# Kernel tuning notes

Hardware: AMD Instinct MI355X
Metric: run time of the kernel (lower is better)

The kernel has to match this reference:

```python
import jax, jax.numpy as jnp
import numpy as np
import math

B = 2        # batch
S = 4095     # input sequence (cls token makes L = 4096)
F_IN = 32    # input feature size
D = 512      # d_model (hidden_size)
H = 8        # n_heads
E = D // H   # head dim = 64
DFF = 2048   # feedforward dim
NL = 2       # encoder layers
FACTOR = 5   # probsparse sampling factor
EPS = 1e-5


def setup_inputs() -> dict:
    key = jax.random.key(0)
    ks = jax.random.split(key, 16)

    def w(k, shape):
        return jax.random.normal(k, shape, dtype=jnp.float32) * 0.02

    inp = {}
    inp['x'] = jax.random.normal(ks[0], (B, S, F_IN), dtype=jnp.float32)
    inp['We'] = w(ks[1], (D, F_IN)); inp['be'] = jnp.zeros((D,), jnp.float32)
    inp['cls'] = jnp.zeros((1, 1, D), jnp.float32)
    inp['Wq'] = w(ks[2], (NL, D, D)); inp['bq'] = jnp.zeros((NL, D), jnp.float32)
    inp['Wk'] = w(ks[3], (NL, D, D)); inp['bk'] = jnp.zeros((NL, D), jnp.float32)
    inp['Wv'] = w(ks[4], (NL, D, D)); inp['bv'] = jnp.zeros((NL, D), jnp.float32)
    inp['Wo'] = w(ks[5], (NL, D, D)); inp['bo'] = jnp.zeros((NL, D), jnp.float32)
    inp['g1'] = jnp.ones((NL, D), jnp.float32); inp['b1'] = jnp.zeros((NL, D), jnp.float32)
    inp['g2'] = jnp.ones((NL, D), jnp.float32); inp['b2'] = jnp.zeros((NL, D), jnp.float32)
    inp['W1'] = w(ks[6], (NL, DFF, D)); inp['bf1'] = jnp.zeros((NL, DFF), jnp.float32)
    inp['W2'] = w(ks[7], (NL, D, DFF)); inp['bf2'] = jnp.zeros((NL, D), jnp.float32)
    inp['Wf'] = w(ks[8], (1, D)); inp['bf'] = jnp.zeros((1,), jnp.float32)
    return inp


def pos_encoding(L):
    # Sinusoidal positional encoding [L, D]
    pos = jnp.arange(L, dtype=jnp.float32)[:, None]
    div = jnp.exp(jnp.arange(0, D, 2, dtype=jnp.float32) * (-math.log(10000.0) / D))
    pe = jnp.zeros((L, D), jnp.float32)
    pe = pe.at[:, 0::2].set(jnp.sin(pos * div))
    pe = pe.at[:, 1::2].set(jnp.cos(pos * div))
    return pe


def layer_norm(x, g, b):
    mu = x.mean(-1, keepdims=True)
    var = ((x - mu) ** 2).mean(-1, keepdims=True)
    return (x - mu) / jnp.sqrt(var + EPS) * g + b


def prob_attention(q, k, v, rng):
    # q, k, v: [B, H, L, E]; mask_flag=False (encoder self-attention)
    b, h, L, e = q.shape
    u = min(FACTOR * int(np.ceil(np.log(L))), L)  # sample_k == n_top here (L_Q == L_K)
    idx = jax.random.randint(rng, (L, u), 0, L)   # random K sampling per query position
    Ks = k[:, :, idx, :]                          # [B,H,L,u,E] gather
    QKs = jnp.einsum('bhle,bhlue->bhlu', q, Ks)   # sampled scores
    M = QKs.max(-1) - QKs.sum(-1) / L             # sparsity measure [B,H,L]
    _, top = jax.lax.top_k(M, u)                  # active query indices [B,H,u]
    Qr = jnp.take_along_axis(q, top[..., None], axis=2)      # [B,H,u,E]
    scores = jnp.einsum('bhue,bhke->bhuk', Qr, k) / math.sqrt(e)
    attn = jax.nn.softmax(scores, axis=-1)
    ctx = jnp.broadcast_to(v.mean(axis=2, keepdims=True), (b, h, L, e))  # initial context = mean(V)
    upd = jnp.einsum('bhuk,bhke->bhue', attn, v)
    bi = jnp.arange(b)[:, None, None]
    hi = jnp.arange(h)[None, :, None]
    ctx = ctx.at[bi, hi, top].set(upd)            # scatter active-query contexts
    return ctx                                    # [B,H,L,E]


def attention_layer(x, Wq_, bq_, Wk_, bk_, Wv_, bv_, Wo_, bo_, rng):
    b, L, _ = x.shape
    q = (x @ Wq_.T + bq_).reshape(b, L, H, E).transpose(0, 2, 1, 3)
    k = (x @ Wk_.T + bk_).reshape(b, L, H, E).transpose(0, 2, 1, 3)
    v = (x @ Wv_.T + bv_).reshape(b, L, H, E).transpose(0, 2, 1, 3)
    ctx = prob_attention(q, k, v, rng)            # [B,H,L,E]
    out = ctx.transpose(0, 2, 1, 3).reshape(b, L, D)
    return out @ Wo_.T + bo_


def reference(x, We, be, cls, Wq, bq, Wk, bk, Wv, bv, Wo, bo, g1, b1, g2, b2, W1, bf1, W2, bf2, Wf, bf):
    h = x @ We.T + be                                            # [B,S,D]
    h = jnp.concatenate([jnp.broadcast_to(cls, (B, 1, D)), h], axis=1)  # prepend cls
    L = h.shape[1]
    h = h + pos_encoding(L)[None]
    for l in range(NL):
        rng = jax.random.fold_in(jax.random.key(42), l)
        a = attention_layer(h, Wq[l], bq[l], Wk[l], bk[l], Wv[l], bv[l], Wo[l], bo[l], rng)
        h = layer_norm(h + a, g1[l], b1[l])
        y = jax.nn.relu(h @ W1[l].T + bf1[l])
        y = y @ W2[l].T + bf2[l]
        h = layer_norm(h + y, g2[l], b2[l])
    return h[:, 0] @ Wf.T + bf  # cls-token prediction head [B,1]
```

## Files before the change

kernel.cpp:

```cpp
#include <hip/hip_runtime.h>
#include <hip/hip_bf16.h>
#include <math.h>
#include <stdint.h>

#define B 2
#define S 4095
#define LSEQ 4096
#define F_IN 32
#define D 512
#define H 8
#define E 64
#define DFF 2048
#define NL 2
#define U 45
#define EPSL 1e-5f
#define LU (LSEQ * U)
#define HALF_LU (LU / 2)
#define NS 32
#define SLICE 128

typedef __attribute__((ext_vector_type(8))) short short8;
typedef __attribute__((ext_vector_type(4))) float f32x4;

#define GLD(gp, lp)                                                            \
    __builtin_amdgcn_global_load_lds(                                          \
        (const __attribute__((address_space(1))) void*)(gp),                   \
        (__attribute__((address_space(3))) void*)(lp), 16, 0, 0)

__device__ __forceinline__ unsigned short bf16_bits(float f) {
    __hip_bfloat16 h = __float2bfloat16(f);
    return *(unsigned short*)&h;
}
__device__ __forceinline__ float bits_to_f32(unsigned short s) {
    union { uint32_t u; float f; } c;
    c.u = ((uint32_t)s) << 16;
    return c.f;
}
__device__ __forceinline__ unsigned long long mkey(float v, int index) {
    uint32_t u = __float_as_uint(v);
    uint32_t mono = (u & 0x80000000u) ? ~u : (u | 0x80000000u);
    return ((unsigned long long)mono << 32) | (uint32_t)(0xFFFFFFFFu - (uint32_t)index);
}

#define TF_BODY(k0, k1, c0, c1, o0, o1)                                        \
    do {                                                                       \
        uint32_t ks2 = (k0) ^ (k1) ^ 0x1BD11BDAu;                              \
        uint32_t x0 = (c0) + (k0), x1 = (c1) + (k1);                           \
        x0 += x1; x1 = ((x1 << 13) | (x1 >> 19)); x1 ^= x0;                    \
        x0 += x1; x1 = ((x1 << 15) | (x1 >> 17)); x1 ^= x0;                    \
        x0 += x1; x1 = ((x1 << 26) | (x1 >> 6));  x1 ^= x0;                    \
        x0 += x1; x1 = ((x1 << 6) | (x1 >> 26));  x1 ^= x0;                    \
        x0 += (k1); x1 += ks2 + 1u;                                            \
        x0 += x1; x1 = ((x1 << 17) | (x1 >> 15)); x1 ^= x0;                    \
        x0 += x1; x1 = ((x1 << 29) | (x1 >> 3));  x1 ^= x0;                    \
        x0 += x1; x1 = ((x1 << 16) | (x1 >> 16)); x1 ^= x0;                    \
        x0 += x1; x1 = ((x1 << 24) | (x1 >> 8));  x1 ^= x0;                    \
        x0 += ks2; x1 += (k0) + 2u;                                            \
        x0 += x1; x1 = ((x1 << 13) | (x1 >> 19)); x1 ^= x0;                    \
        x0 += x1; x1 = ((x1 << 15) | (x1 >> 17)); x1 ^= x0;                    \
        x0 += x1; x1 = ((x1 << 26) | (x1 >> 6));  x1 ^= x0;                    \
        x0 += x1; x1 = ((x1 << 6) | (x1 >> 26));  x1 ^= x0;                    \
        x0 += (k0); x1 += (k1) + 3u;                                           \
        x0 += x1; x1 = ((x1 << 17) | (x1 >> 15)); x1 ^= x0;                    \
        x0 += x1; x1 = ((x1 << 29) | (x1 >> 3));  x1 ^= x0;                    \
        x0 += x1; x1 = ((x1 << 16) | (x1 >> 16)); x1 ^= x0;                    \
        x0 += x1; x1 = ((x1 << 24) | (x1 >> 8));  x1 ^= x0;                    \
        x0 += (k1); x1 += ks2 + 4u;                                            \
        x0 += x1; x1 = ((x1 << 13) | (x1 >> 19)); x1 ^= x0;                    \
        x0 += x1; x1 = ((x1 << 15) | (x1 >> 17)); x1 ^= x0;                    \
        x0 += x1; x1 = ((x1 << 26) | (x1 >> 6));  x1 ^= x0;                    \
        x0 += x1; x1 = ((x1 << 6) | (x1 >> 26));  x1 ^= x0;                    \
        x0 += ks2; x1 += (k0) + 5u;                                            \
        (o0) = x0; (o1) = x1;                                                  \
    } while (0)

__device__ __forceinline__ void threefry_dev(uint32_t k0, uint32_t k1, uint32_t c0,
                                             uint32_t c1, uint32_t& o0, uint32_t& o1) {
    TF_BODY(k0, k1, c0, c1, o0, o1);
}
static void threefry_host(uint32_t k0, uint32_t k1, uint32_t c0, uint32_t c1,
                          uint32_t& o0, uint32_t& o1) {
    TF_BODY(k0, k1, c0, c1, o0, o1);
}

__global__ void prep_embed_kernel(const float* __restrict__ x, const float* __restrict__ We,
                                  __hip_bfloat16* __restrict__ xbf,
                                  __hip_bfloat16* __restrict__ webf) {
    int u = blockIdx.x * blockDim.x + threadIdx.x;
    const int NX = B * LSEQ * F_IN / 4;
    const int NW = D * F_IN / 4;
    if (u < NX) {
        int e0 = u * 4;
        int i = e0 & 31;
        int l = (e0 >> 5) & (LSEQ - 1);
        int b = e0 >> 17;
        union { unsigned short s[4]; uint2 w; } o;
        if (l == 0) {
            o.s[0] = o.s[1] = o.s[2] = o.s[3] = 0;
        } else {
            float4 v = *(const float4*)(x + ((size_t)b * S + (l - 1)) * F_IN + i);
            o.s[0] = bf16_bits(v.x); o.s[1] = bf16_bits(v.y);
            o.s[2] = bf16_bits(v.z); o.s[3] = bf16_bits(v.w);
        }
        ((uint2*)xbf)[u] = o.w;
    } else if (u < NX + NW) {
        int w = u - NX;
        float4 v = ((const float4*)We)[w];
        union { unsigned short s[4]; uint2 w2; } o;
        o.s[0] = bf16_bits(v.x); o.s[1] = bf16_bits(v.y);
        o.s[2] = bf16_bits(v.z); o.s[3] = bf16_bits(v.w);
        ((uint2*)webf)[w] = o.w2;
    }
}

__global__ __launch_bounds__(256) void gemm32(const unsigned short* __restrict__ A,
                                              const unsigned short* __restrict__ W,
                                              const float* __restrict__ bias,
                                              float* __restrict__ Cf,
                                              int M, int N, int K) {
    __shared__ unsigned short lds[2 * 128 * 32];
    unsigned short* As = lds;
    unsigned short* Bs = lds + 128 * 32;
    const int tid = threadIdx.x;
    const int m0 = blockIdx.y * 128, n0 = blockIdx.x * 128;
    const int wave = tid >> 6, lane = tid & 63;
    const int wm = (wave >> 1) * 64, wn = (wave & 1) * 64;
    const int quad = lane >> 4, m15 = lane & 15;
    const int srow = tid >> 2, scol = (tid & 3) * 8;
    f32x4 acc[4][4] = {};
    const unsigned short* Ag0 = A + (size_t)(m0 + srow) * K + scol;
    const unsigned short* Ag1 = A + (size_t)(m0 + srow + 64) * K + scol;
    const unsigned short* Wg0 = W + (size_t)(n0 + srow) * K + scol;
    const unsigned short* Wg1 = W + (size_t)(n0 + srow + 64) * K + scol;
    for (int k0 = 0; k0 < K; k0 += 32) {
        __syncthreads();
        GLD(Ag0 + k0, As + tid * 8);
        GLD(Ag1 + k0, As + 2048 + tid * 8);
        GLD(Wg0 + k0, Bs + tid * 8);
        GLD(Wg1 + k0, Bs + 2048 + tid * 8);
        __syncthreads();
        short8 af[4], bfr[4];
#pragma unroll
        for (int mi = 0; mi < 4; ++mi)
            af[mi] = *(const short8*)(As + (wm + mi * 16 + m15) * 32 + quad * 8);
#pragma unroll
        for (int ni = 0; ni < 4; ++ni)
            bfr[ni] = *(const short8*)(Bs + (wn + ni * 16 + m15) * 32 + quad * 8);
#pragma unroll
        for (int mi = 0; mi < 4; ++mi)
#pragma unroll
            for (int ni = 0; ni < 4; ++ni)
                acc[mi][ni] = __builtin_amdgcn_mfma_f32_16x16x32_bf16(
                    af[mi], bfr[ni], acc[mi][ni], 0, 0, 0);
    }
#pragma unroll
    for (int mi = 0; mi < 4; ++mi) {
        int mg = m0 + wm + mi * 16 + quad * 4;
#pragma unroll
        for (int ni = 0; ni < 4; ++ni) {
            int ng = n0 + wn + ni * 16 + m15;
            float bv = bias[ng];
#pragma unroll
            for (int r = 0; r < 4; ++r)
                Cf[(size_t)(mg + r) * N + ng] = acc[mi][ni][r] + bv;
        }
    }
}

__global__ void posenc_kernel(const float* __restrict__ emb, const float* __restrict__ cls,
                              __hip_bfloat16* __restrict__ hbf) {
    int gid = blockIdx.x * blockDim.x + threadIdx.x;
    if (gid >= B * LSEQ * D) return;
    int d = gid % D;
    int l = (gid / D) % LSEQ;
    float v = (l == 0) ? cls[d] : emb[gid];
    int i = d >> 1;
    float divv = expf((float)(2 * i) * (float)(-9.210340371976184 / 512.0));
    float ang = (float)l * divv;
    v += (d & 1) ? cosf(ang) : sinf(ang);
    hbf[gid] = __float2bfloat16(v);
}

__global__ void cast_weights_kernel(const float* __restrict__ Wq_l,
                                    const float* __restrict__ Wk_l,
                                    const float* __restrict__ Wv_l,
                                    const float* __restrict__ Wo_l,
                                    const float* __restrict__ W1_l,
                                    const float* __restrict__ W2_l,
                                    const float* __restrict__ bq_l,
                                    const float* __restrict__ bk_l,
                                    const float* __restrict__ bv_l,
                                    __hip_bfloat16* __restrict__ wqb,
                                    __hip_bfloat16* __restrict__ wkb,
                                    __hip_bfloat16* __restrict__ wvb,
                                    __hip_bfloat16* __restrict__ wob,
                                    __hip_bfloat16* __restrict__ w1b,
                                    __hip_bfloat16* __restrict__ w2b,
                                    float* __restrict__ qkvbias,
                                    unsigned char* __restrict__ flags) {
    const int SDD = D * D / 4;
    const int SFD = DFF * D / 4;
    const int CAST_N = 4 * SDD + 2 * SFD;
    int u = blockIdx.x * blockDim.x + threadIdx.x;
    if (u >= CAST_N) {
        int j = u - CAST_N;
        if (j < 384) {
            int seg = (j * 4) >> 9;
            int off = (j * 4) & 511;
            const float* src = (seg == 0) ? bq_l : (seg == 1) ? bk_l : bv_l;
            *(float4*)(qkvbias + j * 4) = *(const float4*)(src + off);
        } else if (j < 384 + B * LSEQ / 4) {
            ((int*)flags)[j - 384] = 0;
        }
        return;
    }
    const float* src;
    __hip_bfloat16* dst;
    int off;
    if (u < SDD) { src = Wq_l; dst = wqb; off = u; }
    else if (u < 2 * SDD) { src = Wk_l; dst = wkb; off = u - SDD; }
    else if (u < 3 * SDD) { src = Wv_l; dst = wvb; off = u - 2 * SDD; }
    else if (u < 4 * SDD) { src = Wo_l; dst = wob; off = u - 3 * SDD; }
    else if (u < 4 * SDD + SFD) { src = W1_l; dst = w1b; off = u - 4 * SDD; }
    else { src = W2_l; dst = w2b; off = u - 4 * SDD - SFD; }
    float4 v = ((const float4*)src)[off];
    union { unsigned short s[4]; uint2 w; } o;
    o.s[0] = bf16_bits(v.x); o.s[1] = bf16_bits(v.y);
    o.s[2] = bf16_bits(v.z); o.s[3] = bf16_bits(v.w);
    ((uint2*)dst)[off] = o.w;
}

template <int MODE>
__global__ __launch_bounds__(256) void gemm_pipe(const unsigned short* __restrict__ A,
                                                 const unsigned short* __restrict__ W,
                                                 const float* __restrict__ bias,
                                                 void* __restrict__ C0,
                                                 void* __restrict__ C1,
                                                 void* __restrict__ C2,
                                                 int M, int N, int K, int NBN) {
    __shared__ unsigned short As[2][128 * 32];
    __shared__ unsigned short Bs[2][128 * 32];
    const int tid = threadIdx.x;
    const int NBM = M >> 7;
    const int bid = blockIdx.x;
    const int xcd = bid & 7, local = bid >> 3;
    const int m_t = xcd * (NBM >> 3) + local / NBN;
    const int n_t = local % NBN;
    const int m0 = m_t * 128, n0 = n_t * 128;
    const int wave = tid >> 6, lane = tid & 63;
    const int wm = (wave >> 1) * 64, wn = (wave & 1) * 64;
    const int quad = lane >> 4, m15 = lane & 15;
    const int srow = tid >> 2, scol = (tid & 3) * 8;
    f32x4 acc[4][4] = {};
    const unsigned short* Ag0 = A + (size_t)(m0 + srow) * K + scol;
    const unsigned short* Ag1 = A + (size_t)(m0 + srow + 64) * K + scol;
    const unsigned short* Wg0 = W + (size_t)(n0 + srow) * K + scol;
    const unsigned short* Wg1 = W + (size_t)(n0 + srow + 64) * K + scol;
    GLD(Ag0, As[0] + tid * 8);
    GLD(Ag1, As[0] + 2048 + tid * 8);
    GLD(Wg0, Bs[0] + tid * 8);
    GLD(Wg1, Bs[0] + 2048 + tid * 8);
    int cur = 0;
    for (int k0 = 0; k0 < K; k0 += 32) {
        __syncthreads();
        int kn = k0 + 32;
        if (kn < K) {
            GLD(Ag0 + kn, As[cur ^ 1] + tid * 8);
            GLD(Ag1 + kn, As[cur ^ 1] + 2048 + tid * 8);
            GLD(Wg0 + kn, Bs[cur ^ 1] + tid * 8);
            GLD(Wg1 + kn, Bs[cur ^ 1] + 2048 + tid * 8);
        }
        short8 af[4], bfr[4];
#pragma unroll
        for (int mi = 0; mi < 4; ++mi)
            af[mi] = *(const short8*)(As[cur] + (wm + mi * 16 + m15) * 32 + quad * 8);
#pragma unroll
        for (int ni = 0; ni < 4; ++ni)
            bfr[ni] = *(const short8*)(Bs[cur] + (wn + ni * 16 + m15) * 32 + quad * 8);
#pragma unroll
        for (int mi = 0; mi < 4; ++mi)
#pragma unroll
            for (int ni = 0; ni < 4; ++ni)
                acc[mi][ni] = __builtin_amdgcn_mfma_f32_16x16x32_bf16(
                    af[mi], bfr[ni], acc[mi][ni], 0, 0, 0);
        cur ^= 1;
    }
#pragma unroll
    for (int mi = 0; mi < 4; ++mi) {
        int mg = m0 + wm + mi * 16 + quad * 4;
#pragma unroll
        for (int ni = 0; ni < 4; ++ni) {
            int ng = n0 + wn + ni * 16 + m15;
            float bv = bias[ng];
#pragma unroll
            for (int r = 0; r < 4; ++r) {
                float v = acc[mi][ni][r] + bv;
                if (MODE == 1) {
                    ((__hip_bfloat16*)C0)[(size_t)(mg + r) * N + ng] = __float2bfloat16(v);
                } else if (MODE == 2) {
                    ((__hip_bfloat16*)C0)[(size_t)(mg + r) * N + ng] =
                        __float2bfloat16(fmaxf(v, 0.f));
                } else {
                    int seg = ng >> 9;
                    int col = ng & 511;
                    __hip_bfloat16* dst = (seg == 0) ? (__hip_bfloat16*)C0
                                        : (seg == 1) ? (__hip_bfloat16*)C1
                                                     : (__hip_bfloat16*)C2;
                    dst[(size_t)(mg + r) * D + col] = __float2bfloat16(v);
                }
            }
        }
    }
}

__global__ __launch_bounds__(256) void gemm64_pipe(const unsigned short* __restrict__ A,
                                                   const unsigned short* __restrict__ W,
                                                   const float* __restrict__ bias,
                                                   float* __restrict__ Cf,
                                                   int M, int N, int K, int NBN) {
    __shared__ unsigned short As[2][64 * 32];
    __shared__ unsigned short Bs[2][128 * 32];
    const int tid = threadIdx.x;
    const int NBM = M >> 6;
    const int bid = blockIdx.x;
    const int xcd = bid & 7, local = bid >> 3;
    const int m_t = xcd * (NBM >> 3) + local / NBN;
    const int n_t = local % NBN;
    const int m0 = m_t * 64, n0 = n_t * 128;
    const int wave = tid >> 6, lane = tid & 63;
    const int quad = lane >> 4, m15 = lane & 15;
    const int srow = tid >> 2, scol = (tid & 3) * 8;
    f32x4 acc[8] = {};
    const unsigned short* Ag0 = A + (size_t)(m0 + srow) * K + scol;
    const unsigned short* Wg0 = W + (size_t)(n0 + srow) * K + scol;
    const unsigned short* Wg1 = W + (size_t)(n0 + srow + 64) * K + scol;
    GLD(Ag0, As[0] + tid * 8);
    GLD(Wg0, Bs[0] + tid * 8);
    GLD(Wg1, Bs[0] + 2048 + tid * 8);
    int cur = 0;
    for (int k0 = 0; k0 < K; k0 += 32) {
        __syncthreads();
        int kn = k0 + 32;
        if (kn < K) {
            GLD(Ag0 + kn, As[cur ^ 1] + tid * 8);
            GLD(Wg0 + kn, Bs[cur ^ 1] + tid * 8);
            GLD(Wg1 + kn, Bs[cur ^ 1] + 2048 + tid * 8);
        }
        short8 af = *(const short8*)(As[cur] + (wave * 16 + m15) * 32 + quad * 8);
#pragma unroll
        for (int ni = 0; ni < 8; ++ni) {
            short8 bfr = *(const short8*)(Bs[cur] + (ni * 16 + m15) * 32 + quad * 8);
            acc[ni] = __builtin_amdgcn_mfma_f32_16x16x32_bf16(af, bfr, acc[ni], 0, 0, 0);
        }
        cur ^= 1;
    }
    int mg = m0 + wave * 16 + quad * 4;
#pragma unroll
    for (int ni = 0; ni < 8; ++ni) {
        int ng = n0 + ni * 16 + m15;
        float bv = bias[ng];
#pragma unroll
        for (int r = 0; r < 4; ++r)
            Cf[(size_t)(mg + r) * N + ng] = acc[ni][r] + bv;
    }
}

__global__ __launch_bounds__(256) void mscore_kernel(const __hip_bfloat16* __restrict__ qbf,
                                                     const __hip_bfloat16* __restrict__ kbf,
                                                     uint32_t k2a, uint32_t k2b,
                                                     float* __restrict__ Mv) {
    __shared__ float Sbuf[U][8];
    __shared__ int sidx[U];
    int bid = blockIdx.x;
    int b = bid & 1;
    int l = bid >> 1;
    int tid = threadIdx.x;
    int wave = tid >> 6, lane = tid & 63;
    if (tid < U) {
        int i = l * U + tid;
        uint32_t c0 = (i < HALF_LU) ? (uint32_t)i : (uint32_t)(i - HALF_LU);
        uint32_t o0, o1;
        threefry_dev(k2a, k2b, c0, c0 + HALF_LU, o0, o1);
        sidx[tid] = (int)(((i < HALF_LU) ? o0 : o1) & 4095u);
    }
    const unsigned short* qr =
        (const unsigned short*)qbf + ((size_t)(b * LSEQ) + l) * D + lane * 8;
    union { uint4 u; unsigned short s[8]; } qv;
    qv.u = *(const uint4*)qr;
    float qa[8];
#pragma unroll
    for (int j = 0; j < 8; ++j) qa[j] = bits_to_f32(qv.s[j]);
    __syncthreads();
    const unsigned short* kbase = (const unsigned short*)(kbf + (size_t)(b * LSEQ) * D);
    for (int t = wave; t < U; t += 4) {
        int kr = sidx[t];
        union { uint4 u; unsigned short s[8]; } kv;
        kv.u = *(const uint4*)(kbase + (size_t)kr * D + lane * 8);
        float p = 0.f;
#pragma unroll
        for (int j = 0; j < 8; ++j) p += qa[j] * bits_to_f32(kv.s[j]);
        p += __shfl_xor(p, 1);
        p += __shfl_xor(p, 2);
        p += __shfl_xor(p, 4);
        if ((lane & 7) == 0) Sbuf[t][lane >> 3] = p;
    }
    __syncthreads();
    if (tid < 8) {
        float mx = -INFINITY, sm = 0.f;
        for (int t = 0; t < U; ++t) {
            float v = Sbuf[t][tid];
            mx = fmaxf(mx, v);
            sm += v;
        }
        Mv[((size_t)b * H + tid) * LSEQ + l] = mx - sm / (float)LSEQ;
    }
}

__global__ __launch_bounds__(256) void topk_chunk_kernel(const float* __restrict__ Mv,
                                                         unsigned long long* __restrict__ cand) {
    __shared__ unsigned long long sk[256];
    int blk = blockIdx.x;
    int chunk = blk & 15, bh = blk >> 4;
    int tid = threadIdx.x;
    int gi = chunk * 256 + tid;
    sk[tid] = mkey(Mv[(size_t)bh * LSEQ + gi], gi);
    __syncthreads();
    for (int k = 2; k <= 256; k <<= 1) {
        for (int j = k >> 1; j > 0; j >>= 1) {
            int ixj = tid ^ j;
            if (ixj > tid) {
                unsigned long long a = sk[tid], b = sk[ixj];
                bool desc = ((tid & k) == 0);
                if (desc ? (a < b) : (a > b)) { sk[tid] = b; sk[ixj] = a; }
            }
            __syncthreads();
        }
    }
    if (tid < U) cand[((size_t)bh * 16 + chunk) * U + tid] = sk[tid];
}

__global__ __launch_bounds__(256) void topk_merge_kernel(const unsigned long long* __restrict__ cand,
                                                         int* __restrict__ top) {
    __shared__ unsigned long long sk[1024];
    int bh = blockIdx.x;
    int tid = threadIdx.x;
    for (int e = tid; e < 1024; e += 256)
        sk[e] = (e < 16 * U) ? cand[(size_t)bh * 16 * U + e] : 0ull;
    __syncthreads();
    for (int k = 2; k <= 1024; k <<= 1) {
        for (int j = k >> 1; j > 0; j >>= 1) {
            for (int e = tid; e < 1024; e += 256) {
                int ixj = e ^ j;
                if (ixj > e) {
                    unsigned long long a = sk[e], b = sk[ixj];
                    bool desc = ((e & k) == 0);
                    if (desc ? (a < b) : (a > b)) { sk[e] = b; sk[ixj] = a; }
                }
            }
            __syncthreads();
        }
    }
    if (tid < U)
        top[bh * U + tid] = (int)(0xFFFFFFFFu - (uint32_t)(sk[tid] & 0xFFFFFFFFu));
}

__global__ __launch_bounds__(256) void vmean_part(const __hip_bfloat16* __restrict__ v,
                                                  float* __restrict__ part) {
    int blk = blockIdx.x;
    int seg = blk & 7, hh = (blk >> 3) & 7, b = blk >> 6;
    int e = threadIdx.x & 63, rg = threadIdx.x >> 6;
    const __hip_bfloat16* vp =
        v + ((size_t)(b * LSEQ) + seg * 512) * D + hh * 64 + e;
    float acc = 0.f;
    for (int r = rg; r < 512; r += 4) acc += __bfloat162float(vp[(size_t)r * D]);
    __shared__ float red[4][64];
    red[rg][e] = acc;
    __syncthreads();
    if (threadIdx.x < 64)
        part[(size_t)blk * 64 + threadIdx.x] =
            red[0][threadIdx.x] + red[1][threadIdx.x] + red[2][threadIdx.x] + red[3][threadIdx.x];
}

__global__ void vmean_reduce(const float* __restrict__ part, float* __restrict__ vm) {
    int gid = blockIdx.x * blockDim.x + threadIdx.x;
    if (gid >= B * H * E) return;
    int e = gid & 63, bh = gid >> 6;
    float acc = 0.f;
#pragma unroll
    for (int s = 0; s < 8; ++s) acc += part[((size_t)bh * 8 + s) * 64 + e];
    vm[gid] = acc / (float)LSEQ;
}

__global__ __launch_bounds__(256) void wo_base_kernel(const float* __restrict__ vm,
                                                      const unsigned short* __restrict__ wob,
                                                      const float* __restrict__ bo,
                                                      float* __restrict__ base) {
    int b = blockIdx.x >> 7;
    int n = (blockIdx.x & 127) * 4 + (threadIdx.x >> 6);
    int lane = threadIdx.x & 63;
    const float* vmr = vm + (size_t)b * D + lane * 8;
    float4 va = *(const float4*)vmr;
    float4 vb = *(const float4*)(vmr + 4);
    union { uint4 u; unsigned short s[8]; } w;
    w.u = *(const uint4*)(wob + (size_t)n * D + lane * 8);
    float p = va.x * bits_to_f32(w.s[0]) + va.y * bits_to_f32(w.s[1]) +
              va.z * bits_to_f32(w.s[2]) + va.w * bits_to_f32(w.s[3]) +
              vb.x * bits_to_f32(w.s[4]) + vb.y * bits_to_f32(w.s[5]) +
              vb.z * bits_to_f32(w.s[6]) + vb.w * bits_to_f32(w.s[7]);
    for (int off = 32; off; off >>= 1) p += __shfl_xor(p, off);
    if (lane == 0) base[(size_t)b * D + n] = p + bo[n];
}

__global__ __launch_bounds__(128) void zero_corr_kernel(const int* __restrict__ top,
                                                        float* __restrict__ aout,
                                                        unsigned char* __restrict__ flags) {
    int bid = blockIdx.x;
    int t = bid % U;
    int bh = bid / U;
    int b = bh >> 3;
    int r = top[bh * U + t];
    int tid = threadIdx.x;
    float4 z = {0.f, 0.f, 0.f, 0.f};
    ((float4*)(aout + (size_t)(b * LSEQ + r) * D))[tid] = z;
    if (tid == 0) flags[b * LSEQ + r] = 1;
}

__global__ __launch_bounds__(256) void attnred_corr_kernel(const float* __restrict__ Opart,
                                                           const float* __restrict__ msum,
                                                           const float* __restrict__ vm,
                                                           const unsigned short* __restrict__ wob,
                                                           const int* __restrict__ top,
                                                           float* __restrict__ aout) {
    __shared__ float dlt[E];
    int bid = blockIdx.x;
    int t = bid % U;
    int bh = bid / U;
    int b = bh >> 3, hh = bh & 7;
    int tid = threadIdx.x;
    if (tid < 64) {
        int lane = tid;
        float m_s = -INFINITY, ss = 0.f;
        if (lane < NS) {
            size_t base = (((size_t)bh * NS + lane) * U + t) * 2;
            m_s = msum[base];
            ss = msum[base + 1];
        }
        float M = m_s;
        for (int off = 32; off; off >>= 1) M = fmaxf(M, __shfl_xor(M, off));
        float e_s = (lane < NS) ? __expf(m_s - M) : 0.f;
        float d = ss * e_s;
        for (int off = 32; off; off >>= 1) d += __shfl_xor(d, off);
        float acc = 0.f;
        for (int s = 0; s < NS; ++s) {
            float w = __shfl(e_s, s);
            acc += w * Opart[(((size_t)bh * NS + s) * U + t) * 64 + lane];
        }
        dlt[lane] = acc / d - vm[(size_t)bh * E + lane];
    }
    __syncthreads();
    int r = top[bh * U + t];
    float* arow = aout + (size_t)(b * LSEQ + r) * D;
    for (int n = tid; n < D; n += 256) {
        const unsigned short* wr = wob + (size_t)n * D + hh * E;
        float acc = 0.f;
#pragma unroll
        for (int k2 = 0; k2 < E; ++k2) acc += dlt[k2] * bits_to_f32(wr[k2]);
        atomicAdd(arow + n, acc);
    }
}

__global__ __launch_bounds__(256) void attn_part(const __hip_bfloat16* __restrict__ qbf,
                                                 const __hip_bfloat16* __restrict__ kbf,
                                                 const __hip_bfloat16* __restrict__ vbf,
                                                 const int* __restrict__ top,
                                                 float* __restrict__ Opart,
                                                 float* __restrict__ msum) {
    __shared__ unsigned short Qs[48 * 72];
    __shared__ unsigned short Ks[SLICE * 72];
    __shared__ unsigned short Vs[SLICE * 68];
    __shared__ unsigned short Ps[48 * 136];
    __shared__ float mred[48][4];
    __shared__ float sred[48][4];
    const int slice = blockIdx.x, hh = blockIdx.y, b = blockIdx.z;
    const int bh = b * H + hh;
    const int tid = threadIdx.x;
    const int s0 = slice * SLICE;
    for (int i = tid; i < 48 * 64; i += 256) {
        int t = i >> 6, e = i & 63;
        unsigned short v = 0;
        if (t < U) {
            int r = top[bh * U + t];
            v = ((const unsigned short*)qbf)[((size_t)(b * LSEQ) + r) * D + hh * E + e];
        }
        Qs[t * 72 + e] = v;
    }
    {
        const uint4* src = (const uint4*)(kbf + ((size_t)(b * LSEQ) + s0) * D + hh * E);
        for (int i = tid; i < SLICE * 8; i += 256) {
            int r = i >> 3, c = i & 7;
            uint4 d = src[(size_t)r * 64 + c];
            *(uint4*)(Ks + r * 72 + c * 8) = d;
        }
    }
    {
        const uint2* src = (const uint2*)(vbf + ((size_t)(b * LSEQ) + s0) * D + hh * E);
        for (int i = tid; i < SLICE * 16; i += 256) {
            int r = i >> 4, c = i & 15;
            uint2 d = src[(size_t)r * 128 + c];
            *(uint2*)(Vs + r * 68 + c * 4) = d;
        }
    }
    __syncthreads();
    const int wave = tid >> 6, lane = tid & 63;
    const int quad = lane >> 4, m15 = lane & 15;
    const int wc = wave * 32;
    f32x4 acc[3][2] = {};
#pragma unroll
    for (int ks = 0; ks < 2; ++ks) {
        short8 af[3], bfr[2];
#pragma unroll
        for (int mt = 0; mt < 3; ++mt)
            af[mt] = *(const short8*)(Qs + (mt * 16 + m15) * 72 + ks * 32 + quad * 8);
#pragma unroll
        for (int nt = 0; nt < 2; ++nt)
            bfr[nt] = *(const short8*)(Ks + (wc + nt * 16 + m15) * 72 + ks * 32 + quad * 8);
#pragma unroll
        for (int mt = 0; mt < 3; ++mt)
#pragma unroll
            for (int nt = 0; nt < 2; ++nt)
                acc[mt][nt] = __builtin_amdgcn_mfma_f32_16x16x32_bf16(
                    af[mt], bfr[nt], acc[mt][nt], 0, 0, 0);
    }
    float sc[3][2][4];
#pragma unroll
    for (int mt = 0; mt < 3; ++mt)
#pragma unroll
        for (int nt = 0; nt < 2; ++nt)
#pragma unroll
            for (int r = 0; r < 4; ++r) sc[mt][nt][r] = acc[mt][nt][r] * 0.125f;
#pragma unroll
    for (int mt = 0; mt < 3; ++mt)
#pragma unroll
        for (int r = 0; r < 4; ++r) {
            float mv = fmaxf(sc[mt][0][r], sc[mt][1][r]);
            mv = fmaxf(mv, __shfl_xor(mv, 1));
            mv = fmaxf(mv, __shfl_xor(mv, 2));
            mv = fmaxf(mv, __shfl_xor(mv, 4));
            mv = fmaxf(mv, __shfl_xor(mv, 8));
            if (m15 == 0) mred[mt * 16 + quad * 4 + r][wave] = mv;
        }
    __syncthreads();
#pragma unroll
    for (int mt = 0; mt < 3; ++mt)
#pragma unroll
        for (int r = 0; r < 4; ++r) {
            int row = mt * 16 + quad * 4 + r;
            float ms = fmaxf(fmaxf(mred[row][0], mred[row][1]),
                             fmaxf(mred[row][2], mred[row][3]));
            float p0 = __expf(sc[mt][0][r] - ms);
            float p1 = __expf(sc[mt][1][r] - ms);
            float sv = p0 + p1;
            sv += __shfl_xor(sv, 1);
            sv += __shfl_xor(sv, 2);
            sv += __shfl_xor(sv, 4);
            sv += __shfl_xor(sv, 8);
            if (m15 == 0) sred[row][wave] = sv;
            Ps[row * 136 + wc + m15] = bf16_bits(p0);
            Ps[row * 136 + wc + 16 + m15] = bf16_bits(p1);
        }
    __syncthreads();
    if (tid < U) {
        float mm = fmaxf(fmaxf(mred[tid][0], mred[tid][1]),
                         fmaxf(mred[tid][2], mred[tid][3]));
        float ss = sred[tid][0] + sred[tid][1] + sred[tid][2] + sred[tid][3];
        size_t base = (((size_t)bh * NS + slice) * U + tid) * 2;
        msum[base] = mm;
        msum[base + 1] = ss;
    }
    f32x4 apv[3] = {};
#pragma unroll
    for (int ks = 0; ks < 4; ++ks) {
        short8 bv;
#pragma unroll
        for (int j = 0; j < 8; ++j)
            bv[j] = (short)Vs[(ks * 32 + quad * 8 + j) * 68 + wave * 16 + m15];
        short8 af2[3];
#pragma unroll
        for (int mt = 0; mt < 3; ++mt)
            af2[mt] = *(const short8*)(Ps + (mt * 16 + m15) * 136 + ks * 32 + quad * 8);
#pragma unroll
        for (int mt = 0; mt < 3; ++mt)
            apv[mt] = __builtin_amdgcn_mfma_f32_16x16x32_bf16(af2[mt], bv, apv[mt], 0, 0, 0);
    }
    size_t obase = ((size_t)bh * NS + slice) * U;
#pragma unroll
    for (int mt = 0; mt < 3; ++mt)
#pragma unroll
        for (int r = 0; r < 4; ++r) {
            int row = mt * 16 + quad * 4 + r;
            if (row < U)
                Opart[(obase + row) * 64 + wave * 16 + m15] = apv[mt][r];
        }
}

__global__ __launch_bounds__(64) void add_ln_base_kernel(__hip_bfloat16* __restrict__ hbf,
                                                         const float* __restrict__ base,
                                                         const float* __restrict__ aout,
                                                         const unsigned char* __restrict__ flags,
                                                         const float* __restrict__ g,
                                                         const float* __restrict__ bb) {
    int row = blockIdx.x;
    int b = row >> 12;
    int lane = threadIdx.x;
    unsigned short* hp = (unsigned short*)hbf + (size_t)row * D;
    const float* bp = base + (size_t)b * D;
    const float* ap = aout + (size_t)row * D;
    bool has = flags[row] != 0;
    float x[8];
    float sum = 0.f;
#pragma unroll
    for (int j = 0; j < 8; ++j) {
        float a = bp[lane + 64 * j];
        if (has) a += ap[lane + 64 * j];
        x[j] = bits_to_f32(hp[lane + 64 * j]) + a;
        sum += x[j];
    }
    for (int off = 32; off; off >>= 1) sum += __shfl_xor(sum, off);
    float mu = sum / (float)D;
    float vs = 0.f;
#pragma unroll
    for (int j = 0; j < 8; ++j) {
        float dd = x[j] - mu;
        vs += dd * dd;
    }
    for (int off = 32; off; off >>= 1) vs += __shfl_xor(vs, off);
    float inv = 1.f / sqrtf(vs / (float)D + EPSL);
#pragma unroll
    for (int j = 0; j < 8; ++j) {
        float o = (x[j] - mu) * inv * g[lane + 64 * j] + bb[lane + 64 * j];
        hp[lane + 64 * j] = bf16_bits(o);
    }
}

__global__ __launch_bounds__(64) void add_ln_kernel(__hip_bfloat16* __restrict__ hbf,
                                                    const float* __restrict__ a,
                                                    const float* __restrict__ g,
                                                    const float* __restrict__ bb) {
    int row = blockIdx.x;
    int lane = threadIdx.x;
    unsigned short* hp = (unsigned short*)hbf + (size_t)row * D;
    const float* ap = a + (size_t)row * D;
    float x[8];
    float sum = 0.f;
#pragma unroll
    for (int j = 0; j < 8; ++j) {
        x[j] = bits_to_f32(hp[lane + 64 * j]) + ap[lane + 64 * j];
        sum += x[j];
    }
    for (int off = 32; off; off >>= 1) sum += __shfl_xor(sum, off);
    float mu = sum / (float)D;
    float vs = 0.f;
#pragma unroll
    for (int j = 0; j < 8; ++j) {
        float dd = x[j] - mu;
        vs += dd * dd;
    }
    for (int off = 32; off; off >>= 1) vs += __shfl_xor(vs, off);
    float inv = 1.f / sqrtf(vs / (float)D + EPSL);
#pragma unroll
    for (int j = 0; j < 8; ++j) {
        float o = (x[j] - mu) * inv * g[lane + 64 * j] + bb[lane + 64 * j];
        hp[lane + 64 * j] = bf16_bits(o);
    }
}

__global__ void final_kernel(const __hip_bfloat16* __restrict__ hbf,
                             const float* __restrict__ Wf,
                             const float* __restrict__ bf, float* __restrict__ out) {
    int b = blockIdx.x;
    int lane = threadIdx.x;
    const unsigned short* hp = (const unsigned short*)hbf + (size_t)b * LSEQ * D;
    float acc = 0.f;
    for (int j = lane; j < D; j += 64) acc += bits_to_f32(hp[j]) * Wf[j];
    for (int off = 32; off; off >>= 1) acc += __shfl_xor(acc, off);
    if (lane == 0) out[b] = acc + bf[0];
}

extern "C" void kernel_launch(void* const* d_in, const int* in_sizes, int n_in,
                              void* d_out, int out_size, void* d_ws, size_t ws_size,
                              hipStream_t stream) {
    (void)in_sizes; (void)n_in; (void)out_size; (void)ws_size;
    const float* x   = (const float*)d_in[0];
    const float* We  = (const float*)d_in[1];
    const float* be  = (const float*)d_in[2];
    const float* cls = (const float*)d_in[3];
    const float* Wq  = (const float*)d_in[4];
    const float* bq  = (const float*)d_in[5];
    const float* Wk  = (const float*)d_in[6];
    const float* bk  = (const float*)d_in[7];
    const float* Wv  = (const float*)d_in[8];
    const float* bv  = (const float*)d_in[9];
    const float* Wo  = (const float*)d_in[10];
    const float* bo  = (const float*)d_in[11];
    const float* g1  = (const float*)d_in[12];
    const float* b1  = (const float*)d_in[13];
    const float* g2  = (const float*)d_in[14];
    const float* b2  = (const float*)d_in[15];
    const float* W1  = (const float*)d_in[16];
    const float* bf1 = (const float*)d_in[17];
    const float* W2  = (const float*)d_in[18];
    const float* bf2 = (const float*)d_in[19];
    const float* Wf  = (const float*)d_in[20];
    const float* bff = (const float*)d_in[21];
    float* out = (float*)d_out;

    float* ws = (float*)d_ws;
    const size_t NT = (size_t)B * LSEQ * D;
    float* aout = ws + NT;
    __hip_bfloat16* kbf    = (__hip_bfloat16*)(ws + NT);
    __hip_bfloat16* q_bf   = (__hip_bfloat16*)(ws + 2 * NT);
    __hip_bfloat16* y1_bf  = (__hip_bfloat16*)(ws + 2 * NT);
    __hip_bfloat16* v_bf   = (__hip_bfloat16*)(ws + 4 * NT);
    __hip_bfloat16* h_bf   = (__hip_bfloat16*)(ws + 5 * NT);
    float* emb  = ws;
    float* Opart = ws + 3 * NT;
    float* msumb = Opart + (size_t)B * H * NS * U * 64;
    float* wpool = ws + 5 * NT + NT / 2;
    __hip_bfloat16* wqb = (__hip_bfloat16*)wpool;
    __hip_bfloat16* wkb = wqb + (size_t)D * D;
    __hip_bfloat16* wvb = wkb + (size_t)D * D;
    __hip_bfloat16* wob = wvb + (size_t)D * D;
    __hip_bfloat16* w1b = wob + (size_t)D * D;
    __hip_bfloat16* w2b = w1b + (size_t)DFF * D;
    float* after_w = wpool + ((size_t)4 * D * D + 2 * (size_t)DFF * D) / 2;
    float* Mbuf = after_w;
    int* top    = (int*)(Mbuf + (size_t)B * H * LSEQ);
    float* vm   = (float*)(top + B * H * U);
    float* vpart  = vm + (size_t)B * H * E;
    float* baseb  = vpart + (size_t)128 * 64;
    __hip_bfloat16* xbf  = (__hip_bfloat16*)(baseb + (size_t)B * D);
    __hip_bfloat16* webf = xbf + (size_t)B * LSEQ * F_IN;
    unsigned long long* cand =
        (unsigned long long*)(((uintptr_t)(webf + (size_t)D * F_IN) + 7) & ~(uintptr_t)7);
    float* qkvbias = (float*)(cand + (size_t)B * H * 16 * U);
    unsigned char* flags = (unsigned char*)(qkvbias + 1536);

    const int ML = B * LSEQ;
    dim3 gD(D / 128, ML / 128);
    const int CAST_N = 4 * (D * D / 4) + 2 * (DFF * D / 4);
    const int CAST_TOT = CAST_N + 384 + B * LSEQ / 4;

    prep_embed_kernel<<<(B * LSEQ * F_IN / 4 + D * F_IN / 4 + 255) / 256, 256, 0, stream>>>(
        x, We, xbf, webf);
    gemm32<<<gD, 256, 0, stream>>>((const unsigned short*)xbf,
                                   (const unsigned short*)webf, be, emb, ML, D, F_IN);
    posenc_kernel<<<(B * LSEQ * D + 255) / 256, 256, 0, stream>>>(emb, cls, h_bf);

    for (int l = 0; l < NL; ++l) {
        uint32_t f0, f1, a0, a1, bb0, bb1;
        threefry_host(0u, 42u, 0u, (uint32_t)l, f0, f1);
        threefry_host(f0, f1, 0u, 2u, a0, a1);
        threefry_host(f0, f1, 1u, 3u, bb0, bb1);
        (void)a0; (void)bb0;

        cast_weights_kernel<<<(CAST_TOT + 255) / 256, 256, 0, stream>>>(
            Wq + (size_t)l * D * D, Wk + (size_t)l * D * D, Wv + (size_t)l * D * D,
            Wo + (size_t)l * D * D, W1 + (size_t)l * DFF * D, W2 + (size_t)l * D * DFF,
            bq + l * D, bk + l * D, bv + l * D,
            wqb, wkb, wvb, wob, w1b, w2b, qkvbias, flags);

        gemm_pipe<3><<<768, 256, 0, stream>>>((const unsigned short*)h_bf,
                                              (const unsigned short*)wqb, qkvbias,
                                              q_bf, kbf, v_bf, ML, 3 * D, D, 12);

        mscore_kernel<<<B * LSEQ, 256, 0, stream>>>(q_bf, kbf, a1, bb1, Mbuf);
        topk_chunk_kernel<<<B * H * 16, 256, 0, stream>>>(Mbuf, cand);
        topk_merge_kernel<<<B * H, 256, 0, stream>>>(cand, top);
        vmean_part<<<B * H * 8, 256, 0, stream>>>(v_bf, vpart);
        vmean_reduce<<<4, 256, 0, stream>>>(vpart, vm);
        wo_base_kernel<<<B * 128, 256, 0, stream>>>(vm, (const unsigned short*)wob,
                                                    bo + l * D, baseb);
        attn_part<<<dim3(NS, H, B), 256, 0, stream>>>(q_bf, kbf, v_bf, top, Opart, msumb);
        zero_corr_kernel<<<B * H * U, 128, 0, stream>>>(top, aout, flags);
        attnred_corr_kernel<<<B * H * U, 256, 0, stream>>>(Opart, msumb, vm,
                                                           (const unsigned short*)wob, top,
                                                           aout);
        add_ln_base_kernel<<<ML, 64, 0, stream>>>(h_bf, baseb, aout, flags,
                                                  g1 + l * D, b1 + l * D);

        gemm_pipe<2><<<1024, 256, 0, stream>>>((const unsigned short*)h_bf,
                                               (const unsigned short*)w1b, bf1 + l * DFF,
                                               y1_bf, nullptr, nullptr, ML, DFF, D, 16);
        gemm64_pipe<<<512, 256, 0, stream>>>((const unsigned short*)y1_bf,
                                             (const unsigned short*)w2b, bf2 + l * D,
                                             aout, ML, D, DFF, 4);
        add_ln_kernel<<<ML, 64, 0, stream>>>(h_bf, aout, g2 + l * D, b2 + l * D);
    }

    final_kernel<<<B, 64, 0, stream>>>(h_bf, Wf, bff, out);
}
```

Before: 632.2 us.

## Retile W2 GEMM to 128x128 with split-K and fuse partial sum into LayerNorm

Replaces the 64x128 tile FFN down-projection GEMM with a 128x128 tile kernel using a 2x2 wave layout, a 64-wide K step with XOR-swizzled shared memory, and a two-way split-K. Each half writes its own fp32 partial buffer, and add_ln now sums both partials. The larger tiles raise MFMA work per shared-memory load, and split-K keeps the grid at 512 blocks. The cost is an extra fp32 partial buffer written and read, which reuses the emb workspace region, plus more registers per thread.

```diff
diff --git a/kernel.cpp b/kernel.cpp
--- a/kernel.cpp
+++ b/kernel.cpp
@@ -313,55 +313,83 @@
     }
 }
 
-__global__ __launch_bounds__(256) void gemm64_pipe(const unsigned short* __restrict__ A,
-                                                   const unsigned short* __restrict__ W,
-                                                   const float* __restrict__ bias,
-                                                   float* __restrict__ Cf,
-                                                   int M, int N, int K, int NBN) {
-    __shared__ unsigned short As[2][64 * 32];
-    __shared__ unsigned short Bs[2][128 * 32];
+__global__ __launch_bounds__(256) void gemm_w2(const unsigned short* __restrict__ A,
+                                               const unsigned short* __restrict__ W,
+                                               const float* __restrict__ bias,
+                                               float* __restrict__ C0,
+                                               float* __restrict__ C1) {
+    const int K = 2048, N = 512;
+    __shared__ unsigned short As[2][128 * 64];
+    __shared__ unsigned short Bs[2][128 * 64];
     const int tid = threadIdx.x;
-    const int NBM = M >> 6;
     const int bid = blockIdx.x;
     const int xcd = bid & 7, local = bid >> 3;
-    const int m_t = xcd * (NBM >> 3) + local / NBN;
-    const int n_t = local % NBN;
-    const int m0 = m_t * 64, n0 = n_t * 128;
+    const int m_t = xcd * 8 + (local >> 3);
+    const int n_t = (local >> 1) & 3;
+    const int ks = local & 1;
+    const int m0 = m_t * 128, n0 = n_t * 128;
+    const int kbase = ks * 1024;
     const int wave = tid >> 6, lane = tid & 63;
+    const int wm = (wave >> 1) * 64, wn = (wave & 1) * 64;
     const int quad = lane >> 4, m15 = lane & 15;
-    const int srow = tid >> 2, scol = (tid & 3) * 8;
-    f32x4 acc[8] = {};
-    const unsigned short* Ag0 = A + (size_t)(m0 + srow) * K + scol;
-    const unsigned short* Wg0 = W + (size_t)(n0 + srow) * K + scol;
-    const unsigned short* Wg1 = W + (size_t)(n0 + srow + 64) * K + scol;
-    GLD(Ag0, As[0] + tid * 8);
-    GLD(Wg0, Bs[0] + tid * 8);
-    GLD(Wg1, Bs[0] + 2048 + tid * 8);
+    const int srow = tid >> 3;
+    const int scol = (((tid & 7) ^ (tid >> 3)) & 7) * 8;
+    const unsigned short* Ag = A + (size_t)(m0 + srow) * K + kbase + scol;
+    const unsigned short* Wg = W + (size_t)(n0 + srow) * K + kbase + scol;
+    f32x4 acc[4][4] = {};
+#define STAGE_W2(buf, koff)                                                    \
+    do {                                                                       \
+        GLD(Ag + (koff), As[buf] + tid * 8);                                   \
+        GLD(Ag + (size_t)32 * K + (koff), As[buf] + (tid + 256) * 8);          \
+        GLD(Ag + (size_t)64 * K + (koff), As[buf] + (tid + 512) * 8);          \
+        GLD(Ag + (size_t)96 * K + (koff), As[buf] + (tid + 768) * 8);          \
+        GLD(Wg + (koff), Bs[buf] + tid * 8);                                   \
+        GLD(Wg + (size_t)32 * K + (koff), Bs[buf] + (tid + 256) * 8);          \
+        GLD(Wg + (size_t)64 * K + (koff), Bs[buf] + (tid + 512) * 8);          \
+        GLD(Wg + (size_t)96 * K + (koff), Bs[buf] + (tid + 768) * 8);          \
+    } while (0)
+    STAGE_W2(0, 0);
     int cur = 0;
-    for (int k0 = 0; k0 < K; k0 += 32) {
+    for (int it = 0; it < 16; ++it) {
         __syncthreads();
-        int kn = k0 + 32;
-        if (kn < K) {
-            GLD(Ag0 + kn, As[cur ^ 1] + tid * 8);
-            GLD(Wg0 + kn, Bs[cur ^ 1] + tid * 8);
-            GLD(Wg1 + kn, Bs[cur ^ 1] + 2048 + tid * 8);
-        }
-        short8 af = *(const short8*)(As[cur] + (wave * 16 + m15) * 32 + quad * 8);
-#pragma unroll
-        for (int ni = 0; ni < 8; ++ni) {
-            short8 bfr = *(const short8*)(Bs[cur] + (ni * 16 + m15) * 32 + quad * 8);
-            acc[ni] = __builtin_amdgcn_mfma_f32_16x16x32_bf16(af, bfr, acc[ni], 0, 0, 0);
+        if (it + 1 < 16) STAGE_W2(cur ^ 1, (it + 1) * 64);
+#pragma unroll
+        for (int ks2 = 0; ks2 < 2; ++ks2) {
+            short8 af[4], bfr[4];
+#pragma unroll
+            for (int mi = 0; mi < 4; ++mi) {
+                int row = wm + mi * 16 + m15;
+                af[mi] = *(const short8*)(As[cur] + row * 64 +
+                                          (((ks2 * 4 + quad) ^ (m15 & 7)) * 8));
+            }
+#pragma unroll
+            for (int ni = 0; ni < 4; ++ni) {
+                int row = wn + ni * 16 + m15;
+                bfr[ni] = *(const short8*)(Bs[cur] + row * 64 +
+                                           (((ks2 * 4 + quad) ^ (m15 & 7)) * 8));
+            }
+#pragma unroll
+            for (int mi = 0; mi < 4; ++mi)
+#pragma unroll
+                for (int ni = 0; ni < 4; ++ni)
+                    acc[mi][ni] = __builtin_amdgcn_mfma_f32_16x16x32_bf16(
+                        af[mi], bfr[ni], acc[mi][ni], 0, 0, 0);
         }
         cur ^= 1;
     }
-    int mg = m0 + wave * 16 + quad * 4;
-#pragma unroll
-    for (int ni = 0; ni < 8; ++ni) {
-        int ng = n0 + ni * 16 + m15;
-        float bv = bias[ng];
-#pragma unroll
-        for (int r = 0; r < 4; ++r)
-            Cf[(size_t)(mg + r) * N + ng] = acc[ni][r] + bv;
+#undef STAGE_W2
+    float* Cf = ks ? C1 : C0;
+#pragma unroll
+    for (int mi = 0; mi < 4; ++mi) {
+        int mg = m0 + wm + mi * 16 + quad * 4;
+#pragma unroll
+        for (int ni = 0; ni < 4; ++ni) {
+            int ng = n0 + wn + ni * 16 + m15;
+            float bv = ks ? 0.f : bias[ng];
+#pragma unroll
+            for (int r = 0; r < 4; ++r)
+                Cf[(size_t)(mg + r) * N + ng] = acc[mi][ni][r] + bv;
+        }
     }
 }
 
@@ -744,17 +772,19 @@
 
 __global__ __launch_bounds__(64) void add_ln_kernel(__hip_bfloat16* __restrict__ hbf,
                                                     const float* __restrict__ a,
+                                                    const float* __restrict__ a2,
                                                     const float* __restrict__ g,
                                                     const float* __restrict__ bb) {
     int row = blockIdx.x;
     int lane = threadIdx.x;
     unsigned short* hp = (unsigned short*)hbf + (size_t)row * D;
     const float* ap = a + (size_t)row * D;
+    const float* ap2 = a2 + (size_t)row * D;
     float x[8];
     float sum = 0.f;
 #pragma unroll
     for (int j = 0; j < 8; ++j) {
-        x[j] = bits_to_f32(hp[lane + 64 * j]) + ap[lane + 64 * j];
+        x[j] = bits_to_f32(hp[lane + 64 * j]) + ap[lane + 64 * j] + ap2[lane + 64 * j];
         sum += x[j];
     }
     for (int off = 32; off; off >>= 1) sum += __shfl_xor(sum, off);
@@ -823,6 +853,7 @@
     __hip_bfloat16* v_bf   = (__hip_bfloat16*)(ws + 4 * NT);
     __hip_bfloat16* h_bf   = (__hip_bfloat16*)(ws + 5 * NT);
     float* emb  = ws;
+    float* tmp  = ws;
     float* Opart = ws + 3 * NT;
     float* msumb = Opart + (size_t)B * H * NS * U * 64;
     float* wpool = ws + 5 * NT + NT / 2;
@@ -891,10 +922,10 @@
         gemm_pipe<2><<<1024, 256, 0, stream>>>((const unsigned short*)h_bf,
                                                (const unsigned short*)w1b, bf1 + l * DFF,
                                                y1_bf, nullptr, nullptr, ML, DFF, D, 16);
-        gemm64_pipe<<<512, 256, 0, stream>>>((const unsigned short*)y1_bf,
-                                             (const unsigned short*)w2b, bf2 + l * D,
-                                             aout, ML, D, DFF, 4);
-        add_ln_kernel<<<ML, 64, 0, stream>>>(h_bf, aout, g2 + l * D, b2 + l * D);
+        gemm_w2<<<512, 256, 0, stream>>>((const unsigned short*)y1_bf,
+                                         (const unsigned short*)w2b, bf2 + l * D,
+                                         aout, tmp);
+        add_ln_kernel<<<ML, 64, 0, stream>>>(h_bf, aout, tmp, g2 + l * D, b2 + l * D);
     }
 
     final_kernel<<<B, 64, 0, stream>>>(h_bf, Wf, bff, out);
```

New measurement: 622.4 us. Within noise of the previous version (-1.6%).
